# Kernel tuning notes

Hardware: AMD Instinct MI355X
Metric: run time of the kernel (lower is better)

## Reference

```python
import jax, jax.numpy as jnp
import numpy as np

D_MODEL = 1024
NUM_HEADS = 16
D_K = D_MODEL // NUM_HEADS

def setup_inputs() -> dict:
    key = jax.random.key(0)
    ks = jax.random.split(key, 8)
    B, S, D = 2, 2048, D_MODEL
    scale = 1.0 / np.sqrt(D)
    return {
        "X_q": jax.random.normal(ks[0], (B, S, D), dtype=jnp.float32),
        "X_k": jax.random.normal(ks[1], (B, S, D), dtype=jnp.float32),
        "X_v": jax.random.normal(ks[2], (B, S, D), dtype=jnp.float32),
        "W_q": jax.random.normal(ks[3], (D, D), dtype=jnp.float32) * scale,
        "W_k": jax.random.normal(ks[4], (D, D), dtype=jnp.float32) * scale,
        "W_v": jax.random.normal(ks[5], (D, D), dtype=jnp.float32) * scale,
        "W_o": jax.random.normal(ks[6], (D, D), dtype=jnp.float32) * scale,
        "b_o": jnp.zeros((D,), dtype=jnp.float32),
    }

def reference(X_q, X_k, X_v, W_q, W_k, W_v, W_o, b_o):
    B, S, D = X_q.shape
    H, dk = NUM_HEADS, D_K
    # nn.Linear: x @ W.T
    Q = (X_q @ W_q.T).reshape(B, H, S, dk)  # faithful raw view, no transpose
    K = (X_k @ W_k.T).reshape(B, H, S, dk)
    V = (X_v @ W_v.T).reshape(B, H, S, dk)
    A = jnp.einsum("bhqd,bhkd->bhqk", Q, K) / np.sqrt(dk)  # [B,H,S,S]
    A = jax.nn.softmax(A, axis=-1)
    H_cat = jnp.einsum("bhqk,bhkd->bhqd", A, V).reshape(B, S, D)
    return H_cat @ W_o.T + b_o
```

## Files before the change

kernel.cpp:

```cpp
#include <hip/hip_runtime.h>

typedef __bf16 bf16;
typedef bf16 bf16x8 __attribute__((ext_vector_type(8)));
typedef bf16 bf16x4 __attribute__((ext_vector_type(4)));
typedef bf16 bf16x2 __attribute__((ext_vector_type(2)));
typedef float f32x4 __attribute__((ext_vector_type(4)));
typedef float f32x16 __attribute__((ext_vector_type(16)));
typedef int i32x4 __attribute__((ext_vector_type(4)));

#define XSZ 4194304
#define WSZ 1048576
#define KDIM 1024
#define QSCALE 0.1803368801111137f

__device__ __forceinline__ void async16(const bf16* g, bf16* l) {
  __builtin_amdgcn_global_load_lds(
      (const __attribute__((address_space(1))) unsigned int*)g,
      (__attribute__((address_space(3))) unsigned int*)l, 16, 0, 0);
}

__device__ __forceinline__ bf16x8 ld16(const bf16* p) {
  return __builtin_bit_cast(bf16x8, *(const i32x4*)p);
}

__device__ __forceinline__ f32x4 mfma16(bf16x8 a, bf16x8 b, f32x4 c) {
  return __builtin_amdgcn_mfma_f32_16x16x32_bf16(a, b, c, 0, 0, 0);
}
__device__ __forceinline__ f32x16 mfma32(bf16x8 a, bf16x8 b, f32x16 c) {
  return __builtin_amdgcn_mfma_f32_32x32x16_bf16(a, b, c, 0, 0, 0);
}

__device__ __forceinline__ int packbf2(float lo, float hi) {
  bf16x2 t; t[0] = (bf16)lo; t[1] = (bf16)hi;
  return __builtin_bit_cast(int, t);
}

__device__ __forceinline__ float fast_exp2(float x) {
#if __has_builtin(__builtin_amdgcn_exp2f)
  return __builtin_amdgcn_exp2f(x);
#else
  return exp2f(x);
#endif
}


__global__ __launch_bounds__(256) void cast_all(const float* __restrict__ Xq, const float* __restrict__ Xk,
                                                const float* __restrict__ Xv, const float* __restrict__ Wq,
                                                const float* __restrict__ Wk, const float* __restrict__ Wv,
                                                const float* __restrict__ Wo, bf16* __restrict__ dst) {
  size_t i = ((size_t)blockIdx.x * 256 + threadIdx.x) * 8;
  const float* src; size_t off; float scale = 1.0f;
  if (i < XSZ)                { src = Xq; off = i; }
  else if (i < 2 * (size_t)XSZ) { src = Xk; off = i - XSZ; }
  else if (i < 3 * (size_t)XSZ) { src = Xv; off = i - 2 * (size_t)XSZ; }
  else if (i < 3 * (size_t)XSZ + WSZ) { src = Wq; off = i - 3 * (size_t)XSZ; scale = QSCALE; }
  else if (i < 3 * (size_t)XSZ + 2 * (size_t)WSZ) { src = Wk; off = i - 3 * (size_t)XSZ - WSZ; }
  else if (i < 3 * (size_t)XSZ + 3 * (size_t)WSZ) { src = Wv; off = i - 3 * (size_t)XSZ - 2 * (size_t)WSZ; }
  else                        { src = Wo; off = i - 3 * (size_t)XSZ - 3 * (size_t)WSZ; }
  float4 a = *(const float4*)(src + off);
  float4 b = *(const float4*)(src + off + 4);
  bf16x8 o;
  o[0] = (bf16)(a.x * scale); o[1] = (bf16)(a.y * scale);
  o[2] = (bf16)(a.z * scale); o[3] = (bf16)(a.w * scale);
  o[4] = (bf16)(b.x * scale); o[5] = (bf16)(b.y * scale);
  o[6] = (bf16)(b.z * scale); o[7] = (bf16)(b.w * scale);
  *(bf16x8*)(dst + i) = o;
}

__device__ __forceinline__ void gemm_nt_core(const bf16* __restrict__ A, const bf16* __restrict__ Bm,
                                             int m0, int n0, bf16* lds, f32x4 acc[4][4]) {
  const int t = threadIdx.x;
  const int lane = t & 63, wave = t >> 6;
  const int wm = wave & 1, wn = wave >> 1;
  const int quad = lane >> 4, m16 = lane & 15;
  const bf16* gA[2]; int dstc[2];
  #pragma unroll
  for (int j = 0; j < 2; j++) {
    int c = t + j * 256;
    int row = c >> 2;
    int col = ((c & 3) ^ (row & 3)) * 8;
    gA[j] = A + (size_t)(m0 + row) * KDIM + col;
    dstc[j] = c * 8;
  }
  const ptrdiff_t dBA = (Bm + (size_t)n0 * KDIM) - (A + (size_t)m0 * KDIM);
  const int swzA = quad ^ (m16 & 3);
  #pragma unroll
  for (int j = 0; j < 2; j++) {
    async16(gA[j], lds + dstc[j]);
    async16(gA[j] + dBA, lds + 4096 + dstc[j]);
  }
  for (int kt = 0; kt < 32; ++kt) {
    __syncthreads();
    const int cur = (kt & 1) * 8192;
    if (kt + 1 < 32) {
      const int nxt = 8192 - cur;
      #pragma unroll
      for (int j = 0; j < 2; j++) {
        async16(gA[j] + (kt + 1) * 32, lds + nxt + dstc[j]);
        async16(gA[j] + dBA + (kt + 1) * 32, lds + nxt + 4096 + dstc[j]);
      }
    }
    const bf16* As = lds + cur;
    const bf16* Bs = As + 4096;
    bf16x8 af[4], bfv[4];
    #pragma unroll
    for (int i = 0; i < 4; i++)
      af[i] = ld16(As + (wm * 64 + i * 16 + m16) * 32 + swzA * 8);
    #pragma unroll
    for (int i = 0; i < 4; i++)
      bfv[i] = ld16(Bs + (wn * 64 + i * 16 + m16) * 32 + swzA * 8);
    #pragma unroll
    for (int mi = 0; mi < 4; mi++)
      #pragma unroll
      for (int ni = 0; ni < 4; ni++)
        acc[mi][ni] = mfma16(af[mi], bfv[ni], acc[mi][ni]);
  }
}

__global__ __launch_bounds__(256, 4) void proj_gemm(const bf16* __restrict__ xq, const bf16* __restrict__ xk,
                                                 const bf16* __restrict__ xv, const bf16* __restrict__ wq,
                                                 const bf16* __restrict__ wk, const bf16* __restrict__ wv,
                                                 bf16* __restrict__ Qo, bf16* __restrict__ Ko,
                                                 bf16* __restrict__ Vo) {
  __shared__ __align__(16) bf16 lds[2 * 8192];
  const int z = blockIdx.z;
  const bf16* A = (z == 0) ? xq : (z == 1) ? xk : xv;
  const bf16* W = (z == 0) ? wq : (z == 1) ? wk : wv;
  bf16* C = (z == 0) ? Qo : (z == 1) ? Ko : Vo;
  f32x4 acc[4][4];
  #pragma unroll
  for (int i = 0; i < 4; i++)
    #pragma unroll
    for (int j = 0; j < 4; j++) acc[i][j] = (f32x4){0.f, 0.f, 0.f, 0.f};
  gemm_nt_core(A, W, blockIdx.y * 128, blockIdx.x * 128, lds, acc);
  const int lane = threadIdx.x & 63, wave = threadIdx.x >> 6;
  const int wm = wave & 1, wn = wave >> 1, quad = lane >> 4, m16 = lane & 15;
  const int row0 = blockIdx.y * 128 + wm * 64;
  const int col0 = blockIdx.x * 128 + wn * 64;
  #pragma unroll
  for (int mi = 0; mi < 4; mi++)
    #pragma unroll
    for (int ni = 0; ni < 4; ni++)
      #pragma unroll
      for (int r = 0; r < 4; r++) {
        int row = row0 + mi * 16 + quad * 4 + r;
        int col = col0 + ni * 16 + m16;
        C[(size_t)row * 1024 + col] = (bf16)acc[mi][ni][r];
      }
}

__global__ __launch_bounds__(256, 4) void out_gemm(const bf16* __restrict__ Hm, const bf16* __restrict__ wo,
                                                const float* __restrict__ bias, float* __restrict__ out) {
  __shared__ __align__(16) bf16 lds[2 * 6144];
  const int t = threadIdx.x;
  const int lane = t & 63, wave = t >> 6;
  const int wm = wave & 1, wn = wave >> 1;
  const int quad = lane >> 4, m16 = lane & 15;
  const int m0 = blockIdx.y * 128, n0 = blockIdx.x * 64;
  const bf16* gA[2]; int dstA[2];
  #pragma unroll
  for (int j = 0; j < 2; j++) {
    int c = t + j * 256;
    int row = c >> 2;
    int col = ((c & 3) ^ (row & 3)) * 8;
    gA[j] = Hm + (size_t)(m0 + row) * KDIM + col;
    dstA[j] = c * 8;
  }
  const bf16* gB; int dstB;
  {
    int c = t;
    int row = c >> 2;
    int col = ((c & 3) ^ (row & 3)) * 8;
    gB = wo + (size_t)(n0 + row) * KDIM + col;
    dstB = c * 8;
  }
  const int swzA = quad ^ (m16 & 3);
  f32x4 acc[4][2];
  #pragma unroll
  for (int i = 0; i < 4; i++)
    #pragma unroll
    for (int j = 0; j < 2; j++) acc[i][j] = (f32x4){0.f, 0.f, 0.f, 0.f};
  #pragma unroll
  for (int j = 0; j < 2; j++) async16(gA[j], lds + dstA[j]);
  async16(gB, lds + 4096 + dstB);
  for (int kt = 0; kt < 32; ++kt) {
    __syncthreads();
    const int cur = (kt & 1) * 6144;
    if (kt + 1 < 32) {
      const int nxt = 6144 - cur;
      #pragma unroll
      for (int j = 0; j < 2; j++) async16(gA[j] + (kt + 1) * 32, lds + nxt + dstA[j]);
      async16(gB + (kt + 1) * 32, lds + nxt + 4096 + dstB);
    }
    const bf16* As = lds + cur;
    const bf16* Bs = As + 4096;
    bf16x8 af[4], bfv[2];
    #pragma unroll
    for (int i = 0; i < 4; i++)
      af[i] = ld16(As + (wm * 64 + i * 16 + m16) * 32 + swzA * 8);
    #pragma unroll
    for (int i = 0; i < 2; i++)
      bfv[i] = ld16(Bs + (wn * 32 + i * 16 + m16) * 32 + swzA * 8);
    #pragma unroll
    for (int mi = 0; mi < 4; mi++)
      #pragma unroll
      for (int ni = 0; ni < 2; ni++)
        acc[mi][ni] = mfma16(af[mi], bfv[ni], acc[mi][ni]);
  }
  const int row0 = m0 + wm * 64;
  const int col0 = n0 + wn * 32;
  float bv[2];
  #pragma unroll
  for (int ni = 0; ni < 2; ni++) bv[ni] = bias[col0 + ni * 16 + m16];
  #pragma unroll
  for (int mi = 0; mi < 4; mi++)
    #pragma unroll
    for (int ni = 0; ni < 2; ni++)
      #pragma unroll
      for (int r = 0; r < 4; r++) {
        int row = row0 + mi * 16 + quad * 4 + r;
        int col = col0 + ni * 16 + m16;
        out[(size_t)row * 1024 + col] = acc[mi][ni][r] + bv[ni];
      }
}

__global__ __launch_bounds__(256) void transpose_v(const bf16* __restrict__ V, bf16* __restrict__ Vt) {
  __shared__ bf16 T[64 * 65];
  const int t = threadIdx.x;
  const bf16* src = V + (size_t)blockIdx.y * (2048 * 64) + (size_t)blockIdx.x * 64 * 64;
  bf16* dst = Vt + (size_t)blockIdx.y * (2048 * 64) + (size_t)blockIdx.x * 64;
  #pragma unroll
  for (int j = 0; j < 2; j++) {
    int c = t + j * 256;
    int row = c >> 3, col8 = (c & 7) * 8;
    bf16x8 v = *(const bf16x8*)(src + row * 64 + col8);
    #pragma unroll
    for (int i = 0; i < 8; i++) T[row * 65 + col8 + i] = v[i];
  }
  __syncthreads();
  #pragma unroll
  for (int j = 0; j < 2; j++) {
    int c = t + j * 256;
    int d = c >> 3, k8 = (c & 7) * 8;
    bf16x8 o;
    #pragma unroll
    for (int i = 0; i < 8; i++) o[i] = T[(k8 + i) * 65 + d];
    *(bf16x8*)(dst + (size_t)d * 2048 + k8) = o;
  }
}

__global__ __launch_bounds__(512, 2) void attn_kernel(const bf16* __restrict__ Qg,
                                                      const bf16* __restrict__ Kg,
                                                      const bf16* __restrict__ Vtg,
                                                      bf16* __restrict__ Hout) {
  __shared__ __align__(16) bf16 smem[32768];
  const int t = threadIdx.x;
  const int lane = t & 63;
  const int w = (t >> 6) & 3;
  const int half = t >> 8;
  const int tt = t & 255;
  const int l31 = lane & 31, h = lane >> 5, l7 = lane & 7;
  bf16* hb = smem + half * 16384;
  const int L = blockIdx.x + 16 * blockIdx.y;
  const int xcd = L & 7, j5 = L >> 3;
  const int bh = xcd * 4 + (j5 & 3);
  const int qt = j5 >> 2;
  const size_t base = (size_t)bh * (2048 * 64);
  const bf16* Kp = Kg + base;
  const bf16* Vp = Vtg + base;
  const int q = qt * 128 + w * 32 + l31;

  bf16x8 qf[4];
  #pragma unroll
  for (int kc = 0; kc < 4; kc++)
    qf[kc] = *(const bf16x8*)(Qg + base + (size_t)q * 64 + 16 * kc + 8 * h);

  f32x16 oacc[2];
  #pragma unroll
  for (int mt = 0; mt < 2; mt++)
    #pragma unroll
    for (int i = 0; i < 16; i++) oacc[mt][i] = 0.f;
  float lrow = 0.f;

  const bf16* ksrc[2]; const bf16* vsrc[2]; int dstc[2];
  #pragma unroll
  for (int j = 0; j < 2; j++) {
    int c = tt + j * 256;
    int row = c >> 3;
    int sw = ((c & 7) ^ (row & 7)) * 8;
    ksrc[j] = Kp + (size_t)(half * 1024 + row) * 64 + sw;
    vsrc[j] = Vp + (size_t)row * 2048 + half * 1024 + sw;
    dstc[j] = c * 8;
  }

  #pragma unroll
  for (int j = 0; j < 2; j++) {
    async16(ksrc[j], hb + dstc[j]);
    async16(vsrc[j], hb + 4096 + dstc[j]);
  }

  for (int st = 0; st < 16; ++st) {
    __syncthreads();
    const int buf = st & 1;
    if (st + 1 < 16) {
      const int nb = (buf ^ 1) * 8192;
      #pragma unroll
      for (int j = 0; j < 2; j++) {
        async16(ksrc[j] + (st + 1) * 4096, hb + nb + dstc[j]);
        async16(vsrc[j] + (st + 1) * 64,   hb + nb + 4096 + dstc[j]);
      }
    }
    bf16* Kb = hb + buf * 8192;
    bf16* Vb = Kb + 4096;

    #pragma unroll
    for (int mtq = 0; mtq < 2; mtq++) {
      f32x16 sacc;
      #pragma unroll
      for (int i = 0; i < 16; i++) sacc[i] = 0.f;
      #pragma unroll
      for (int kc = 0; kc < 4; kc++) {
        bf16x8 kf = ld16(Kb + (32 * mtq + l31) * 64 + (((2 * kc + h) ^ l7) << 3));
        sacc = mfma32(kf, qf[kc], sacc);
      }
      int pd[8];
      float sum = 0.f;
      #pragma unroll
      for (int p = 0; p < 8; p++) {
        float p0 = fast_exp2(sacc[2 * p]);
        float p1 = fast_exp2(sacc[2 * p + 1]);
        sum += p0 + p1;
        pd[p] = packbf2(p0, p1);
      }
      lrow += sum;
      #pragma unroll
      for (int c1 = 0; c1 < 2; c1++) {
        const int kcp = 2 * mtq + c1;
        const int rro = 2 * c1 + h;
        const int rrp = 2 * c1 + 1 - h;
        int s0 = __shfl_xor(pd[2 * rrp], 32, 64);
        int s1 = __shfl_xor(pd[2 * rrp + 1], 32, 64);
        int o0 = pd[2 * rro], o1 = pd[2 * rro + 1];
        i32x4 w4;
        w4.x = h ? s0 : o0;
        w4.y = h ? s1 : o1;
        w4.z = h ? o0 : s0;
        w4.w = h ? o1 : s1;
        bf16x8 pfrag = __builtin_bit_cast(bf16x8, w4);
        #pragma unroll
        for (int mtd = 0; mtd < 2; mtd++) {
          bf16x8 vf = ld16(Vb + (32 * mtd + l31) * 64 + (((2 * kcp + h) ^ l7) << 3));
          oacc[mtd] = mfma32(vf, pfrag, oacc[mtd]);
        }
      }
    }
  }
  __syncthreads();

  lrow += __shfl_xor(lrow, 32, 64);
  float* Sf = (float*)smem;
  float* Tf = Sf + w * 2048;
  float* Lb = Sf + 8192 + w * 32;
  if (half) {
    #pragma unroll
    for (int mt = 0; mt < 2; mt++)
      #pragma unroll
      for (int r = 0; r < 16; r++) {
        int d = 32 * mt + (r & 3) + 8 * (r >> 2) + 4 * h;
        Tf[d * 32 + l31] = oacc[mt][r];
      }
    if (!h) Lb[l31] = lrow;
  }
  __syncthreads();
  if (!half) {
    float linv = 1.f / (lrow + Lb[l31]);
    #pragma unroll
    for (int mt = 0; mt < 2; mt++)
      #pragma unroll
      for (int r = 0; r < 16; r++) {
        int d = 32 * mt + (r & 3) + 8 * (r >> 2) + 4 * h;
        Tf[d * 32 + l31] = (oacc[mt][r] + Tf[d * 32 + l31]) * linv;
      }
  }
  __syncthreads();
  bf16* Hq = Hout + base + (size_t)(qt * 128 + w * 32 + l31) * 64 + 32 * h;
  #pragma unroll
  for (int s = 0; s < 2; s++) {
    int se = half * 2 + s;
    bf16x8 o;
    #pragma unroll
    for (int i = 0; i < 8; i++) o[i] = (bf16)Tf[(32 * h + se * 8 + i) * 32 + l31];
    *(bf16x8*)(Hq + se * 8) = o;
  }
}

extern "C" void kernel_launch(void* const* d_in, const int* in_sizes, int n_in,
                              void* d_out, int out_size, void* d_ws, size_t ws_size,
                              hipStream_t stream) {
  const float* Xq = (const float*)d_in[0];
  const float* Xk = (const float*)d_in[1];
  const float* Xv = (const float*)d_in[2];
  const float* Wq = (const float*)d_in[3];
  const float* Wk = (const float*)d_in[4];
  const float* Wv = (const float*)d_in[5];
  const float* Wo = (const float*)d_in[6];
  const float* bo = (const float*)d_in[7];

  bf16* ws = (bf16*)d_ws;
  bf16* xq = ws;
  bf16* xk = ws + XSZ;
  bf16* xv = ws + 2 * (size_t)XSZ;
  bf16* wq = ws + 3 * (size_t)XSZ;
  bf16* wk = wq + WSZ;
  bf16* wv = wk + WSZ;
  bf16* wo = wv + WSZ;
  bf16* q  = wo + WSZ;
  bf16* k  = q + XSZ;
  bf16* v  = k + XSZ;
  bf16* vt = xv;
  bf16* h  = xq;

  cast_all<<<8192, 256, 0, stream>>>(Xq, Xk, Xv, Wq, Wk, Wv, Wo, ws);
  proj_gemm<<<dim3(8, 32, 3), 256, 0, stream>>>(xq, xk, xv, wq, wk, wv, q, k, v);
  transpose_v<<<dim3(32, 32), 256, 0, stream>>>(v, vt);
  attn_kernel<<<dim3(16, 32), 512, 0, stream>>>(q, k, vt, h);
  out_gemm<<<dim3(16, 32), 256, 0, stream>>>(h, wo, bo, (float*)d_out);
}
```

Before: 232.5 us.

## Halve attention KV tile to 32 keys to fit four blocks per CU

```diff
diff --git a/kernel.cpp b/kernel.cpp
--- a/kernel.cpp
+++ b/kernel.cpp
@@ -249,18 +249,18 @@
   }
 }
 
-__global__ __launch_bounds__(512, 2) void attn_kernel(const bf16* __restrict__ Qg,
+__global__ __launch_bounds__(512, 4) void attn_kernel(const bf16* __restrict__ Qg,
                                                       const bf16* __restrict__ Kg,
                                                       const bf16* __restrict__ Vtg,
                                                       bf16* __restrict__ Hout) {
-  __shared__ __align__(16) bf16 smem[32768];
+  __shared__ __align__(16) bf16 smem[16640];
   const int t = threadIdx.x;
   const int lane = t & 63;
   const int w = (t >> 6) & 3;
   const int half = t >> 8;
   const int tt = t & 255;
   const int l31 = lane & 31, h = lane >> 5, l7 = lane & 7;
-  bf16* hb = smem + half * 16384;
+  bf16* hb = smem + half * 8192;
   const int L = blockIdx.x + 16 * blockIdx.y;
   const int xcd = L & 7, j5 = L >> 3;
   const int bh = xcd * 4 + (j5 & 3);
@@ -282,76 +282,63 @@
     for (int i = 0; i < 16; i++) oacc[mt][i] = 0.f;
   float lrow = 0.f;
 
-  const bf16* ksrc[2]; const bf16* vsrc[2]; int dstc[2];
-  #pragma unroll
-  for (int j = 0; j < 2; j++) {
-    int c = tt + j * 256;
-    int row = c >> 3;
-    int sw = ((c & 7) ^ (row & 7)) * 8;
-    ksrc[j] = Kp + (size_t)(half * 1024 + row) * 64 + sw;
-    vsrc[j] = Vp + (size_t)row * 2048 + half * 1024 + sw;
-    dstc[j] = c * 8;
-  }
-
-  #pragma unroll
-  for (int j = 0; j < 2; j++) {
-    async16(ksrc[j], hb + dstc[j]);
-    async16(vsrc[j], hb + 4096 + dstc[j]);
-  }
-
-  for (int st = 0; st < 16; ++st) {
+  const int krow = tt >> 3, kg = tt & 7;
+  const int vrow = tt >> 2, vg = tt & 3;
+  const bf16* ksrc = Kp + (size_t)(half * 1024 + krow) * 64 + ((kg ^ (krow & 7)) * 8);
+  const bf16* vsrc = Vp + (size_t)vrow * 2048 + half * 1024 + ((vg ^ (vrow & 3)) * 8);
+  const int kdst = tt * 8;
+  const int vdst = tt * 8;
+
+  async16(ksrc, hb + kdst);
+  async16(vsrc, hb + 2048 + vdst);
+
+  for (int st = 0; st < 32; ++st) {
     __syncthreads();
     const int buf = st & 1;
-    if (st + 1 < 16) {
-      const int nb = (buf ^ 1) * 8192;
-      #pragma unroll
-      for (int j = 0; j < 2; j++) {
-        async16(ksrc[j] + (st + 1) * 4096, hb + nb + dstc[j]);
-        async16(vsrc[j] + (st + 1) * 64,   hb + nb + 4096 + dstc[j]);
-      }
-    }
-    bf16* Kb = hb + buf * 8192;
-    bf16* Vb = Kb + 4096;
-
-    #pragma unroll
-    for (int mtq = 0; mtq < 2; mtq++) {
-      f32x16 sacc;
-      #pragma unroll
-      for (int i = 0; i < 16; i++) sacc[i] = 0.f;
-      #pragma unroll
-      for (int kc = 0; kc < 4; kc++) {
-        bf16x8 kf = ld16(Kb + (32 * mtq + l31) * 64 + (((2 * kc + h) ^ l7) << 3));
-        sacc = mfma32(kf, qf[kc], sacc);
-      }
-      int pd[8];
-      float sum = 0.f;
-      #pragma unroll
-      for (int p = 0; p < 8; p++) {
-        float p0 = fast_exp2(sacc[2 * p]);
-        float p1 = fast_exp2(sacc[2 * p + 1]);
-        sum += p0 + p1;
-        pd[p] = packbf2(p0, p1);
-      }
-      lrow += sum;
-      #pragma unroll
-      for (int c1 = 0; c1 < 2; c1++) {
-        const int kcp = 2 * mtq + c1;
-        const int rro = 2 * c1 + h;
-        const int rrp = 2 * c1 + 1 - h;
-        int s0 = __shfl_xor(pd[2 * rrp], 32, 64);
-        int s1 = __shfl_xor(pd[2 * rrp + 1], 32, 64);
-        int o0 = pd[2 * rro], o1 = pd[2 * rro + 1];
-        i32x4 w4;
-        w4.x = h ? s0 : o0;
-        w4.y = h ? s1 : o1;
-        w4.z = h ? o0 : s0;
-        w4.w = h ? o1 : s1;
-        bf16x8 pfrag = __builtin_bit_cast(bf16x8, w4);
-        #pragma unroll
-        for (int mtd = 0; mtd < 2; mtd++) {
-          bf16x8 vf = ld16(Vb + (32 * mtd + l31) * 64 + (((2 * kcp + h) ^ l7) << 3));
-          oacc[mtd] = mfma32(vf, pfrag, oacc[mtd]);
-        }
+    if (st + 1 < 32) {
+      bf16* nb = hb + (buf ^ 1) * 4096;
+      async16(ksrc + (size_t)(st + 1) * 2048, nb + kdst);
+      async16(vsrc + (size_t)(st + 1) * 32,   nb + 2048 + vdst);
+    }
+    const bf16* Kb = hb + buf * 4096;
+    const bf16* Vb = Kb + 2048;
+
+    f32x16 sacc;
+    #pragma unroll
+    for (int i = 0; i < 16; i++) sacc[i] = 0.f;
+    #pragma unroll
+    for (int kc = 0; kc < 4; kc++) {
+      bf16x8 kf = ld16(Kb + l31 * 64 + (((2 * kc + h) ^ l7) << 3));
+      sacc = mfma32(kf, qf[kc], sacc);
+    }
+    int pd[8];
+    float sum = 0.f;
+    #pragma unroll
+    for (int p = 0; p < 8; p++) {
+      float p0 = fast_exp2(sacc[2 * p]);
+      float p1 = fast_exp2(sacc[2 * p + 1]);
+      sum += p0 + p1;
+      pd[p] = packbf2(p0, p1);
+    }
+    lrow += sum;
+    #pragma unroll
+    for (int c1 = 0; c1 < 2; c1++) {
+      const int rro = 2 * c1 + h;
+      const int rrp = 2 * c1 + 1 - h;
+      int s0 = __shfl_xor(pd[2 * rrp], 32, 64);
+      int s1 = __shfl_xor(pd[2 * rrp + 1], 32, 64);
+      int o0 = pd[2 * rro], o1 = pd[2 * rro + 1];
+      i32x4 w4;
+      w4.x = h ? s0 : o0;
+      w4.y = h ? s1 : o1;
+      w4.z = h ? o0 : s0;
+      w4.w = h ? o1 : s1;
+      bf16x8 pfrag = __builtin_bit_cast(bf16x8, w4);
+      #pragma unroll
+      for (int mtd = 0; mtd < 2; mtd++) {
+        const int row = 32 * mtd + l31;
+        bf16x8 vf = ld16(Vb + row * 32 + (((2 * c1 + h) ^ (row & 3)) << 3));
+        oacc[mtd] = mfma32(vf, pfrag, oacc[mtd]);
       }
     }
   }
```

Result: slower. 252.7 us (+8.7%).
